# Kernel optimization log

Measured on AMD Instinct MI355X. Metric: run time of the kernel, lower is better.

The kernel has to match this reference:

```python
import jax, jax.numpy as jnp
import numpy as np

N = 100000      # nodes
E = 3200000     # edges (avg degree 32)
F = 256         # input features
C = 256         # output channels


def setup_inputs() -> dict:
    key = jax.random.key(0)
    k1, k2, k3, k4, k5 = jax.random.split(key, 5)
    x = jax.random.normal(k1, (N, F), dtype=jnp.float32)
    edge_row = jax.random.randint(k2, (E,), 0, N, dtype=jnp.int32)
    edge_col = jax.random.randint(k3, (E,), 0, N, dtype=jnp.int32)
    # precomputed normalized adjacency values (D^-1/2 (A+I) D^-1/2 entries)
    edge_vals = jax.random.uniform(k4, (E,), dtype=jnp.float32)
    kernel = jax.random.normal(k5, (F, C), dtype=jnp.float32) * (1.0 / np.sqrt(F))
    bias = jnp.zeros((C,), dtype=jnp.float32)
    return {"x": x, "edge_row": edge_row, "edge_col": edge_col,
            "edge_vals": edge_vals, "kernel": kernel, "bias": bias}


def reference(x, edge_row, edge_col, edge_vals, kernel, bias):
    # GraphConv: Z = relu( A_hat @ (X @ W) + b ), single mode, sparse A_hat.
    h = x @ kernel                                   # [N, C]
    msgs = edge_vals[:, None] * h[edge_col]          # [E, C] gather along cols
    agg = jax.ops.segment_sum(msgs, edge_row, num_segments=N)  # [N, C]
    return jax.nn.relu(agg + bias)
```

## Files before the change

### kernel.cpp

```cpp
#include <hip/hip_runtime.h>
#include <hip/hip_bf16.h>
#include <hip/hip_fp16.h>


#define BROWS 128
#define CH_A1 16384
#define CH_A3 8192
#define GEMM_SMEM 10240

typedef __attribute__((ext_vector_type(4))) float f32x4;
typedef __attribute__((ext_vector_type(2))) int i32x2;
typedef __attribute__((ext_vector_type(8))) short s16x8;

__device__ __forceinline__ unsigned short f2bf(float f) {
    unsigned u = __float_as_uint(f);
    u += 0x7FFFu + ((u >> 16) & 1u);
    return (unsigned short)(u >> 16);
}
__device__ __forceinline__ float bf2f(unsigned short s) {
    return __uint_as_float(((unsigned)s) << 16);
}

__device__ __forceinline__ void gemm_body(const float* __restrict__ X,
                                          const unsigned short* __restrict__ Wt,
                                          unsigned short* __restrict__ H,
                                          int M, int g, char* smem) {
    typedef unsigned short AsRow[40];
    AsRow* As = (AsRow*)smem;
    int t = threadIdx.x;
    int lane = t & 63;
    int w = t >> 6;
    int r0 = g * 64;
    int c0 = w * 64;
    int srow = t >> 2;
    int sslot = t & 3;
    int gr = r0 + srow; if (gr >= M) gr = M - 1;

    f32x4 acc[4][4] = {};

    for (int k0 = 0; k0 < 256; k0 += 32) {
        const float* p = &X[(size_t)gr * 256 + k0 + sslot * 8];
        f32x4 a0 = __builtin_nontemporal_load((const f32x4*)p);
        f32x4 a1 = __builtin_nontemporal_load((const f32x4*)(p + 4));
        s16x8 va;
        va[0] = (short)f2bf(a0[0]); va[1] = (short)f2bf(a0[1]);
        va[2] = (short)f2bf(a0[2]); va[3] = (short)f2bf(a0[3]);
        va[4] = (short)f2bf(a1[0]); va[5] = (short)f2bf(a1[1]);
        va[6] = (short)f2bf(a1[2]); va[7] = (short)f2bf(a1[3]);
        __syncthreads();
        *(s16x8*)&As[srow][sslot * 8] = va;
        __syncthreads();

        int kofs = (lane >> 4) * 8;
        s16x8 afr[4], bfr[4];
#pragma unroll
        for (int mi = 0; mi < 4; ++mi)
            afr[mi] = *(const s16x8*)&As[mi * 16 + (lane & 15)][kofs];
#pragma unroll
        for (int ni = 0; ni < 4; ++ni) {
            int cn = c0 + ni * 16 + (lane & 15);
            bfr[ni] = *(const s16x8*)&Wt[(size_t)cn * 256 + k0 + kofs];
        }
#pragma unroll
        for (int mi = 0; mi < 4; ++mi)
#pragma unroll
            for (int ni = 0; ni < 4; ++ni)
                acc[mi][ni] = __builtin_amdgcn_mfma_f32_16x16x32_bf16(
                    afr[mi], bfr[ni], acc[mi][ni], 0, 0, 0);
    }

#pragma unroll
    for (int mi = 0; mi < 4; ++mi) {
#pragma unroll
        for (int ni = 0; ni < 4; ++ni) {
            int rg = r0 + mi * 16 + (lane >> 4) * 4;
            int cg = c0 + ni * 16 + (lane & 15);
#pragma unroll
            for (int j = 0; j < 4; ++j) {
                if (rg + j < M)
                    H[(size_t)(rg + j) * 256 + cg] = f2bf(acc[mi][ni][j]);
            }
        }
    }
}

__device__ __forceinline__ void hist_body(const int* __restrict__ row,
                                          int* __restrict__ gcnt,
                                          int E, int NB, int chunk, char* smem) {
    int* h = (int*)smem;
    int t = threadIdx.x;
    for (int j = t; j < NB; j += 256) h[j] = 0;
    __syncthreads();
    int start = chunk * CH_A1;
    int end = min(E, start + CH_A1);
    for (int i = start + t; i < end; i += 256)
        atomicAdd(&h[row[i] >> 7], 1);
    __syncthreads();
    for (int j = t; j < NB; j += 256)
        if (h[j]) atomicAdd(&gcnt[j], h[j]);
}

__device__ __forceinline__ void a3_body(const int* __restrict__ row,
                                        const int* __restrict__ col,
                                        const float* __restrict__ val,
                                        int* __restrict__ gcur,
                                        int2* __restrict__ binned,
                                        int E, int NB, int chunk, char* smem) {
    int* h    = (int*)smem;
    int* base = h + NB;
    int* cur  = base + NB;
    int t = threadIdx.x;
    for (int j = t; j < NB; j += 256) { h[j] = 0; cur[j] = 0; }
    __syncthreads();
    int start = chunk * CH_A3;
    int end = min(E, start + CH_A3);
    for (int i = start + t; i < end; i += 256)
        atomicAdd(&h[row[i] >> 7], 1);
    __syncthreads();
    for (int j = t; j < NB; j += 256) {
        int c = h[j];
        base[j] = c ? atomicAdd(&gcur[j], c) : 0;
    }
    __syncthreads();
    for (int i = start + t; i < end; i += 256) {
        int r = row[i];
        int b = r >> 7;
        int ofs = atomicAdd(&cur[b], 1);
        unsigned hb = (unsigned)__half_as_ushort(__float2half(val[i]));
        binned[base[b] + ofs] = make_int2(col[i] | (int)(hb << 17), r & (BROWS - 1));
    }
}

__device__ __forceinline__ void kb_body(const int2* __restrict__ binned,
                                        const int* __restrict__ bkt_base,
                                        int* __restrict__ rowptr,
                                        unsigned* __restrict__ csr,
                                        int N, int b, char* smem) {
    int* cnt = (int*)smem;
    int* sc  = cnt + BROWS;
    int* cur = sc + BROWS;
    int t = threadIdx.x;
    int r0 = b * BROWS;
    int bb = bkt_base[b];
    int be = bkt_base[b + 1];
    if (t < BROWS) cnt[t] = 0;
    __syncthreads();
    for (int i = bb + t; i < be; i += 256) {
        i32x2 e = __builtin_nontemporal_load((const i32x2*)&binned[i]);
        atomicAdd(&cnt[e[1]], 1);
    }
    __syncthreads();
    if (t < BROWS) sc[t] = cnt[t];
    __syncthreads();
    for (int off = 1; off < BROWS; off <<= 1) {
        int tmp = (t < BROWS && t >= off) ? sc[t - off] : 0;
        __syncthreads();
        if (t < BROWS && t >= off) sc[t] += tmp;
        __syncthreads();
    }
    if (t < BROWS) {
        int ex = sc[t] - cnt[t];
        cur[t] = ex;
        if (r0 + t < N) rowptr[r0 + t] = bb + ex;
    }
    __syncthreads();
    for (int i = bb + t; i < be; i += 256) {
        i32x2 e = __builtin_nontemporal_load((const i32x2*)&binned[i]);
        int ofs = atomicAdd(&cur[e[1]], 1);
        csr[bb + ofs] = (unsigned)e[0];
    }
}

__global__ __launch_bounds__(1024) void kA2(const int* __restrict__ gcnt,
                                            int* __restrict__ bkt_base,
                                            int* __restrict__ gcur,
                                            int* __restrict__ rowptr,
                                            int NB, int N, int E) {
    __shared__ int s[1024];
    int t = threadIdx.x;
    int v = (t < NB) ? gcnt[t] : 0;
    s[t] = v;
    __syncthreads();
    for (int off = 1; off < 1024; off <<= 1) {
        int tmp = (t >= off) ? s[t - off] : 0;
        __syncthreads();
        if (t >= off) s[t] += tmp;
        __syncthreads();
    }
    if (t < NB) {
        int ex = s[t] - v;
        bkt_base[t] = ex;
        gcur[t] = ex;
    }
    if (t == 0) {
        bkt_base[NB] = E;
        rowptr[N] = E;
    }
}

__global__ __launch_bounds__(256) void h0(const int* __restrict__ row,
                                          int* __restrict__ gcnt,
                                          int E, int NB, int nHist,
                                          const float* __restrict__ W,
                                          unsigned short* __restrict__ Wt) {
    extern __shared__ char smem[];
    int bid = blockIdx.x;
    int t = threadIdx.x;
    if (bid < nHist) { hist_body(row, gcnt, E, NB, bid, smem); return; }
    int idx = (bid - nHist) * 256 + t;
    int k = idx >> 8, c = idx & 255;
    Wt[c * 256 + k] = f2bf(W[idx]);
}

__global__ __launch_bounds__(256) void h1(const int* __restrict__ row,
                                          const int* __restrict__ col,
                                          const float* __restrict__ val,
                                          int* __restrict__ gcur,
                                          int2* __restrict__ binned,
                                          int E, int NB, int nA3,
                                          const float* __restrict__ X,
                                          const unsigned short* __restrict__ Wt,
                                          unsigned short* __restrict__ H,
                                          int M, int g0) {
    extern __shared__ char smem[];
    int bid = blockIdx.x;
    if (bid < nA3) { a3_body(row, col, val, gcur, binned, E, NB, bid, smem); return; }
    gemm_body(X, Wt, H, M, g0 + (bid - nA3), smem);
}

__global__ __launch_bounds__(256) void h2(const int2* __restrict__ binned,
                                          const int* __restrict__ bktb,
                                          int* __restrict__ rowptr,
                                          unsigned* __restrict__ csr,
                                          int N, int NB,
                                          const float* __restrict__ X,
                                          const unsigned short* __restrict__ Wt,
                                          unsigned short* __restrict__ H,
                                          int M, int g0) {
    extern __shared__ char smem[];
    int bid = blockIdx.x;
    if (bid < NB) { kb_body(binned, bktb, rowptr, csr, N, bid, smem); return; }
    gemm_body(X, Wt, H, M, g0 + (bid - NB), smem);
}

__global__ __launch_bounds__(256) void k_gemm_solo(const float* __restrict__ X,
                                                   const unsigned short* __restrict__ Wt,
                                                   unsigned short* __restrict__ H, int M) {
    extern __shared__ char smem[];
    gemm_body(X, Wt, H, M, blockIdx.x, smem);
}

__global__ __launch_bounds__(256) void k_agg(const unsigned short* __restrict__ H,
                                             const int* __restrict__ rowptr,
                                             const unsigned* __restrict__ csr,
                                             const float* __restrict__ bias,
                                             float* __restrict__ out, int n) {
    int wave = threadIdx.x >> 6;
    int lane = threadIdx.x & 63;
    int node = blockIdx.x * 4 + wave;
    if (node >= n) return;
    int s = rowptr[node];
    int e = rowptr[node + 1];
    int h = lane >> 5;
    int cbase = (lane & 31) * 8;

    float a0=0.f,a1=0.f,a2=0.f,a3=0.f,a4=0.f,a5=0.f,a6=0.f,a7=0.f;

#define ACC(K, HV)                                                      \
    {                                                                   \
        float v = __half2float(__ushort_as_half((unsigned short)((K) >> 17))); \
        a0 += v * bf2f((unsigned short)(HV)[0]);                        \
        a1 += v * bf2f((unsigned short)(HV)[1]);                        \
        a2 += v * bf2f((unsigned short)(HV)[2]);                        \
        a3 += v * bf2f((unsigned short)(HV)[3]);                        \
        a4 += v * bf2f((unsigned short)(HV)[4]);                        \
        a5 += v * bf2f((unsigned short)(HV)[5]);                        \
        a6 += v * bf2f((unsigned short)(HV)[6]);                        \
        a7 += v * bf2f((unsigned short)(HV)[7]);                        \
    }

    int i = s;
    for (; i + 7 < e; i += 8) {
        unsigned k0 = csr[i + h];
        unsigned k1 = csr[i + 2 + h];
        unsigned k2 = csr[i + 4 + h];
        unsigned k3 = csr[i + 6 + h];
        s16x8 g0 = *(const s16x8*)&H[(k0 & 0x1FFFFu) * 256 + cbase];
        s16x8 g1 = *(const s16x8*)&H[(k1 & 0x1FFFFu) * 256 + cbase];
        s16x8 g2 = *(const s16x8*)&H[(k2 & 0x1FFFFu) * 256 + cbase];
        s16x8 g3 = *(const s16x8*)&H[(k3 & 0x1FFFFu) * 256 + cbase];
        ACC(k0, g0); ACC(k1, g1); ACC(k2, g2); ACC(k3, g3);
    }
    for (; i + 1 < e; i += 2) {
        unsigned k0 = csr[i + h];
        s16x8 g0 = *(const s16x8*)&H[(k0 & 0x1FFFFu) * 256 + cbase];
        ACC(k0, g0);
    }
    if (i < e) {
        unsigned k0 = csr[i];
        s16x8 g0 = *(const s16x8*)&H[(k0 & 0x1FFFFu) * 256 + cbase];
        float v = h ? 0.f
                    : __half2float(__ushort_as_half((unsigned short)(k0 >> 17)));
        a0 += v * bf2f((unsigned short)g0[0]);
        a1 += v * bf2f((unsigned short)g0[1]);
        a2 += v * bf2f((unsigned short)g0[2]);
        a3 += v * bf2f((unsigned short)g0[3]);
        a4 += v * bf2f((unsigned short)g0[4]);
        a5 += v * bf2f((unsigned short)g0[5]);
        a6 += v * bf2f((unsigned short)g0[6]);
        a7 += v * bf2f((unsigned short)g0[7]);
    }
#undef ACC

    a0 += __shfl_xor(a0, 32); a1 += __shfl_xor(a1, 32);
    a2 += __shfl_xor(a2, 32); a3 += __shfl_xor(a3, 32);
    a4 += __shfl_xor(a4, 32); a5 += __shfl_xor(a5, 32);
    a6 += __shfl_xor(a6, 32); a7 += __shfl_xor(a7, 32);

    float w0 = h ? a4 : a0;
    float w1 = h ? a5 : a1;
    float w2 = h ? a6 : a2;
    float w3 = h ? a7 : a3;
    int cw = cbase + h * 4;
    float4 b4 = *(const float4*)&bias[cw];
    f32x4 o;
    o[0] = fmaxf(w0 + b4.x, 0.f);
    o[1] = fmaxf(w1 + b4.y, 0.f);
    o[2] = fmaxf(w2 + b4.z, 0.f);
    o[3] = fmaxf(w3 + b4.w, 0.f);
    __builtin_nontemporal_store(o, (f32x4*)&out[node * 256 + cw]);
}

extern "C" void kernel_launch(void* const* d_in, const int* in_sizes, int n_in,
                              void* d_out, int out_size, void* d_ws, size_t ws_size,
                              hipStream_t stream) {
    const float* x     = (const float*)d_in[0];
    const int*   erow  = (const int*)d_in[1];
    const int*   ecol  = (const int*)d_in[2];
    const float* evals = (const float*)d_in[3];
    const float* W     = (const float*)d_in[4];
    const float* bias  = (const float*)d_in[5];
    float* out = (float*)d_out;

    const int C = 256;
    const int N = in_sizes[0] / C;
    const int E = in_sizes[1];
    const int NB = (N + BROWS - 1) / BROWS;

    char* ws = (char*)d_ws;
    size_t off = 0;
    auto carve = [&](size_t bytes) -> void* {
        void* p = ws + off;
        off += (bytes + 255) & ~(size_t)255;
        return p;
    };
    unsigned short* Hbf  = (unsigned short*)carve((size_t)N * C * 2);
    unsigned*       csr  = (unsigned*)carve((size_t)E * 4);
    int*            rowp = (int*)carve((size_t)(N + 1) * 4);
    unsigned short* Wt   = (unsigned short*)carve((size_t)C * 256 * 2);
    int*            gcnt = (int*)carve((size_t)NB * 4);
    int*            gcur = (int*)carve((size_t)NB * 4);
    int*            bktb = (int*)carve((size_t)(NB + 1) * 4);

    bool fused = (off + (size_t)E * 8) <= ws_size;
    int2* binned = fused ? (int2*)carve((size_t)E * 8) : (int2*)Hbf;

    int nHist = (E + CH_A1 - 1) / CH_A1;
    int nA3   = (E + CH_A3 - 1) / CH_A3;
    int gemmBlocks = (N + 63) / 64;

    int G1 = fused ? 650 : 0;
    int G2 = fused ? (gemmBlocks - 650) : 0;

    hipMemsetAsync(gcnt, 0, (size_t)NB * 4, stream);
    h0<<<nHist + 256, 256, GEMM_SMEM, stream>>>(erow, gcnt, E, NB, nHist, W, Wt);
    kA2<<<1, 1024, 0, stream>>>(gcnt, bktb, gcur, rowp, NB, N, E);
    h1<<<nA3 + G1, 256, GEMM_SMEM, stream>>>(erow, ecol, evals, gcur, binned,
                                             E, NB, nA3, x, Wt, Hbf, N, 0);
    h2<<<NB + G2, 256, GEMM_SMEM, stream>>>(binned, bktb, rowp, csr, N, NB,
                                            x, Wt, Hbf, N, G1);
    if (!fused)
        k_gemm_solo<<<gemmBlocks, 256, GEMM_SMEM, stream>>>(x, Wt, Hbf, N);

    k_agg<<<(N + 3) / 4, 256, 0, stream>>>(Hbf, rowp, csr, bias, out, N);
}
```

Before: 396.9 us.

## Replace global CSR build with fixed-capacity buckets and fused per-bucket aggregation

```diff
diff --git a/kernel.cpp b/kernel.cpp
--- a/kernel.cpp
+++ b/kernel.cpp
@@ -3,13 +3,12 @@
 #include <hip/hip_fp16.h>
 
 
-#define BROWS 128
-#define CH_A1 16384
+#define CAP 2432
+#define NBMAX 1600
 #define CH_A3 8192
-#define GEMM_SMEM 10240
+#define D1_SMEM 19200
 
 typedef __attribute__((ext_vector_type(4))) float f32x4;
-typedef __attribute__((ext_vector_type(2))) int i32x2;
 typedef __attribute__((ext_vector_type(8))) short s16x8;
 
 __device__ __forceinline__ unsigned short f2bf(float f) {
@@ -19,6 +18,53 @@
 }
 __device__ __forceinline__ float bf2f(unsigned short s) {
     return __uint_as_float(((unsigned)s) << 16);
+}
+
+__global__ __launch_bounds__(256) void k_pre(const float* __restrict__ W,
+                                             unsigned short* __restrict__ Wt,
+                                             int* __restrict__ gcur, int NB) {
+    int bid = blockIdx.x, t = threadIdx.x;
+    if (bid < 256) {
+        int idx = bid * 256 + t;
+        int k = idx >> 8, c = idx & 255;
+        Wt[c * 256 + k] = f2bf(W[idx]);
+    } else {
+        for (int j = t; j < NB; j += 256) gcur[j] = 0;
+    }
+}
+
+__device__ __forceinline__ void a3_body(const int* __restrict__ row,
+                                        const int* __restrict__ col,
+                                        const float* __restrict__ val,
+                                        int* __restrict__ gcur,
+                                        unsigned* __restrict__ bcv,
+                                        unsigned char* __restrict__ blr,
+                                        int E, int NB, int chunk, char* smem) {
+    int* h    = (int*)smem;
+    int* base = h + NBMAX;
+    int* cur  = base + NBMAX;
+    int t = threadIdx.x;
+    for (int j = t; j < NB; j += 256) { h[j] = 0; cur[j] = 0; }
+    __syncthreads();
+    int start = chunk * CH_A3;
+    int end = min(E, start + CH_A3);
+    for (int i = start + t; i < end; i += 256)
+        atomicAdd(&h[row[i] >> 6], 1);
+    __syncthreads();
+    for (int j = t; j < NB; j += 256) {
+        int c = h[j];
+        base[j] = c ? atomicAdd(&gcur[j], c) : 0;
+    }
+    __syncthreads();
+    for (int i = start + t; i < end; i += 256) {
+        int r = row[i];
+        int b = r >> 6;
+        int ofs = atomicAdd(&cur[b], 1);
+        size_t idx = (size_t)b * CAP + base[b] + ofs;
+        unsigned hb = (unsigned)__half_as_ushort(__float2half(val[i]));
+        bcv[idx] = (unsigned)col[i] | (hb << 17);
+        blr[idx] = (unsigned char)(r & 63);
+    }
 }
 
 __device__ __forceinline__ void gemm_body(const float* __restrict__ X,
@@ -84,187 +130,69 @@
     }
 }
 
-__device__ __forceinline__ void hist_body(const int* __restrict__ row,
-                                          int* __restrict__ gcnt,
-                                          int E, int NB, int chunk, char* smem) {
-    int* h = (int*)smem;
-    int t = threadIdx.x;
-    for (int j = t; j < NB; j += 256) h[j] = 0;
-    __syncthreads();
-    int start = chunk * CH_A1;
-    int end = min(E, start + CH_A1);
-    for (int i = start + t; i < end; i += 256)
-        atomicAdd(&h[row[i] >> 7], 1);
-    __syncthreads();
-    for (int j = t; j < NB; j += 256)
-        if (h[j]) atomicAdd(&gcnt[j], h[j]);
-}
-
-__device__ __forceinline__ void a3_body(const int* __restrict__ row,
-                                        const int* __restrict__ col,
-                                        const float* __restrict__ val,
-                                        int* __restrict__ gcur,
-                                        int2* __restrict__ binned,
-                                        int E, int NB, int chunk, char* smem) {
-    int* h    = (int*)smem;
-    int* base = h + NB;
-    int* cur  = base + NB;
-    int t = threadIdx.x;
-    for (int j = t; j < NB; j += 256) { h[j] = 0; cur[j] = 0; }
-    __syncthreads();
-    int start = chunk * CH_A3;
-    int end = min(E, start + CH_A3);
-    for (int i = start + t; i < end; i += 256)
-        atomicAdd(&h[row[i] >> 7], 1);
-    __syncthreads();
-    for (int j = t; j < NB; j += 256) {
-        int c = h[j];
-        base[j] = c ? atomicAdd(&gcur[j], c) : 0;
-    }
-    __syncthreads();
-    for (int i = start + t; i < end; i += 256) {
-        int r = row[i];
-        int b = r >> 7;
-        int ofs = atomicAdd(&cur[b], 1);
-        unsigned hb = (unsigned)__half_as_ushort(__float2half(val[i]));
-        binned[base[b] + ofs] = make_int2(col[i] | (int)(hb << 17), r & (BROWS - 1));
-    }
-}
-
-__device__ __forceinline__ void kb_body(const int2* __restrict__ binned,
-                                        const int* __restrict__ bkt_base,
-                                        int* __restrict__ rowptr,
-                                        unsigned* __restrict__ csr,
-                                        int N, int b, char* smem) {
-    int* cnt = (int*)smem;
-    int* sc  = cnt + BROWS;
-    int* cur = sc + BROWS;
-    int t = threadIdx.x;
-    int r0 = b * BROWS;
-    int bb = bkt_base[b];
-    int be = bkt_base[b + 1];
-    if (t < BROWS) cnt[t] = 0;
-    __syncthreads();
-    for (int i = bb + t; i < be; i += 256) {
-        i32x2 e = __builtin_nontemporal_load((const i32x2*)&binned[i]);
-        atomicAdd(&cnt[e[1]], 1);
-    }
-    __syncthreads();
-    if (t < BROWS) sc[t] = cnt[t];
-    __syncthreads();
-    for (int off = 1; off < BROWS; off <<= 1) {
-        int tmp = (t < BROWS && t >= off) ? sc[t - off] : 0;
-        __syncthreads();
-        if (t < BROWS && t >= off) sc[t] += tmp;
-        __syncthreads();
-    }
-    if (t < BROWS) {
-        int ex = sc[t] - cnt[t];
-        cur[t] = ex;
-        if (r0 + t < N) rowptr[r0 + t] = bb + ex;
-    }
-    __syncthreads();
-    for (int i = bb + t; i < be; i += 256) {
-        i32x2 e = __builtin_nontemporal_load((const i32x2*)&binned[i]);
-        int ofs = atomicAdd(&cur[e[1]], 1);
-        csr[bb + ofs] = (unsigned)e[0];
-    }
-}
-
-__global__ __launch_bounds__(1024) void kA2(const int* __restrict__ gcnt,
-                                            int* __restrict__ bkt_base,
-                                            int* __restrict__ gcur,
-                                            int* __restrict__ rowptr,
-                                            int NB, int N, int E) {
-    __shared__ int s[1024];
-    int t = threadIdx.x;
-    int v = (t < NB) ? gcnt[t] : 0;
-    s[t] = v;
-    __syncthreads();
-    for (int off = 1; off < 1024; off <<= 1) {
-        int tmp = (t >= off) ? s[t - off] : 0;
-        __syncthreads();
-        if (t >= off) s[t] += tmp;
-        __syncthreads();
-    }
-    if (t < NB) {
-        int ex = s[t] - v;
-        bkt_base[t] = ex;
-        gcur[t] = ex;
-    }
-    if (t == 0) {
-        bkt_base[NB] = E;
-        rowptr[N] = E;
-    }
-}
-
-__global__ __launch_bounds__(256) void h0(const int* __restrict__ row,
-                                          int* __restrict__ gcnt,
-                                          int E, int NB, int nHist,
-                                          const float* __restrict__ W,
-                                          unsigned short* __restrict__ Wt) {
+__global__ __launch_bounds__(256) void kD1(const int* __restrict__ row,
+                                           const int* __restrict__ col,
+                                           const float* __restrict__ val,
+                                           int* __restrict__ gcur,
+                                           unsigned* __restrict__ bcv,
+                                           unsigned char* __restrict__ blr,
+                                           int E, int NB, int nA3,
+                                           const float* __restrict__ X,
+                                           const unsigned short* __restrict__ Wt,
+                                           unsigned short* __restrict__ H, int M) {
     extern __shared__ char smem[];
     int bid = blockIdx.x;
+    if (bid < nA3) {
+        a3_body(row, col, val, gcur, bcv, blr, E, NB, bid, smem);
+        return;
+    }
+    gemm_body(X, Wt, H, M, bid - nA3, smem);
+}
+
+__global__ __launch_bounds__(256) void kD2(const unsigned* __restrict__ bcv,
+                                           const unsigned char* __restrict__ blr,
+                                           const int* __restrict__ gcur,
+                                           const unsigned short* __restrict__ H,
+                                           const float* __restrict__ bias,
+                                           float* __restrict__ out, int N) {
+    __shared__ int cnt[64], rs[64], cur[64];
+    __shared__ unsigned csr[CAP];
+    int b = blockIdx.x;
     int t = threadIdx.x;
-    if (bid < nHist) { hist_body(row, gcnt, E, NB, bid, smem); return; }
-    int idx = (bid - nHist) * 256 + t;
-    int k = idx >> 8, c = idx & 255;
-    Wt[c * 256 + k] = f2bf(W[idx]);
-}
-
-__global__ __launch_bounds__(256) void h1(const int* __restrict__ row,
-                                          const int* __restrict__ col,
-                                          const float* __restrict__ val,
-                                          int* __restrict__ gcur,
-                                          int2* __restrict__ binned,
-                                          int E, int NB, int nA3,
-                                          const float* __restrict__ X,
-                                          const unsigned short* __restrict__ Wt,
-                                          unsigned short* __restrict__ H,
-                                          int M, int g0) {
-    extern __shared__ char smem[];
-    int bid = blockIdx.x;
-    if (bid < nA3) { a3_body(row, col, val, gcur, binned, E, NB, bid, smem); return; }
-    gemm_body(X, Wt, H, M, g0 + (bid - nA3), smem);
-}
-
-__global__ __launch_bounds__(256) void h2(const int2* __restrict__ binned,
-                                          const int* __restrict__ bktb,
-                                          int* __restrict__ rowptr,
-                                          unsigned* __restrict__ csr,
-                                          int N, int NB,
-                                          const float* __restrict__ X,
-                                          const unsigned short* __restrict__ Wt,
-                                          unsigned short* __restrict__ H,
-                                          int M, int g0) {
-    extern __shared__ char smem[];
-    int bid = blockIdx.x;
-    if (bid < NB) { kb_body(binned, bktb, rowptr, csr, N, bid, smem); return; }
-    gemm_body(X, Wt, H, M, g0 + (bid - NB), smem);
-}
-
-__global__ __launch_bounds__(256) void k_gemm_solo(const float* __restrict__ X,
-                                                   const unsigned short* __restrict__ Wt,
-                                                   unsigned short* __restrict__ H, int M) {
-    extern __shared__ char smem[];
-    gemm_body(X, Wt, H, M, blockIdx.x, smem);
-}
-
-__global__ __launch_bounds__(256) void k_agg(const unsigned short* __restrict__ H,
-                                             const int* __restrict__ rowptr,
-                                             const unsigned* __restrict__ csr,
-                                             const float* __restrict__ bias,
-                                             float* __restrict__ out, int n) {
-    int wave = threadIdx.x >> 6;
-    int lane = threadIdx.x & 63;
-    int node = blockIdx.x * 4 + wave;
-    if (node >= n) return;
-    int s = rowptr[node];
-    int e = rowptr[node + 1];
+    size_t gb = (size_t)b * CAP;
+    int n = gcur[b];
+
+    if (t < 64) cnt[t] = 0;
+    __syncthreads();
+    for (int i = t; i < n; i += 256)
+        atomicAdd(&cnt[blr[gb + i]], 1);
+    __syncthreads();
+    if (t < 64) rs[t] = cnt[t];
+    __syncthreads();
+    for (int off = 1; off < 64; off <<= 1) {
+        int tmp = (t < 64 && t >= off) ? rs[t - off] : 0;
+        __syncthreads();
+        if (t < 64 && t >= off) rs[t] += tmp;
+        __syncthreads();
+    }
+    if (t < 64) {
+        int ex = rs[t] - cnt[t];
+        rs[t] = ex;
+        cur[t] = ex;
+    }
+    __syncthreads();
+    for (int i = t; i < n; i += 256) {
+        unsigned cv = bcv[gb + i];
+        int lr = blr[gb + i];
+        int ofs = atomicAdd(&cur[lr], 1);
+        csr[ofs] = cv;
+    }
+    __syncthreads();
+
+    int wave = t >> 6;
+    int lane = t & 63;
     int h = lane >> 5;
     int cbase = (lane & 31) * 8;
-
-    float a0=0.f,a1=0.f,a2=0.f,a3=0.f,a4=0.f,a5=0.f,a6=0.f,a7=0.f;
 
 #define ACC(K, HV)                                                      \
     {                                                                   \
@@ -279,56 +207,66 @@
         a7 += v * bf2f((unsigned short)(HV)[7]);                        \
     }
 
-    int i = s;
-    for (; i + 7 < e; i += 8) {
-        unsigned k0 = csr[i + h];
-        unsigned k1 = csr[i + 2 + h];
-        unsigned k2 = csr[i + 4 + h];
-        unsigned k3 = csr[i + 6 + h];
-        s16x8 g0 = *(const s16x8*)&H[(k0 & 0x1FFFFu) * 256 + cbase];
-        s16x8 g1 = *(const s16x8*)&H[(k1 & 0x1FFFFu) * 256 + cbase];
-        s16x8 g2 = *(const s16x8*)&H[(k2 & 0x1FFFFu) * 256 + cbase];
-        s16x8 g3 = *(const s16x8*)&H[(k3 & 0x1FFFFu) * 256 + cbase];
-        ACC(k0, g0); ACC(k1, g1); ACC(k2, g2); ACC(k3, g3);
-    }
-    for (; i + 1 < e; i += 2) {
-        unsigned k0 = csr[i + h];
-        s16x8 g0 = *(const s16x8*)&H[(k0 & 0x1FFFFu) * 256 + cbase];
-        ACC(k0, g0);
-    }
-    if (i < e) {
-        unsigned k0 = csr[i];
-        s16x8 g0 = *(const s16x8*)&H[(k0 & 0x1FFFFu) * 256 + cbase];
-        float v = h ? 0.f
-                    : __half2float(__ushort_as_half((unsigned short)(k0 >> 17)));
-        a0 += v * bf2f((unsigned short)g0[0]);
-        a1 += v * bf2f((unsigned short)g0[1]);
-        a2 += v * bf2f((unsigned short)g0[2]);
-        a3 += v * bf2f((unsigned short)g0[3]);
-        a4 += v * bf2f((unsigned short)g0[4]);
-        a5 += v * bf2f((unsigned short)g0[5]);
-        a6 += v * bf2f((unsigned short)g0[6]);
-        a7 += v * bf2f((unsigned short)g0[7]);
+    for (int rr = 0; rr < 16; ++rr) {
+        int r = wave * 16 + rr;
+        int node = b * 64 + r;
+        if (node >= N) break;
+        int s = rs[r];
+        int e = s + cnt[r];
+
+        float a0=0.f,a1=0.f,a2=0.f,a3=0.f,a4=0.f,a5=0.f,a6=0.f,a7=0.f;
+
+        int i = s;
+        for (; i + 7 < e; i += 8) {
+            unsigned k0 = csr[i + h];
+            unsigned k1 = csr[i + 2 + h];
+            unsigned k2 = csr[i + 4 + h];
+            unsigned k3 = csr[i + 6 + h];
+            s16x8 g0 = *(const s16x8*)&H[(k0 & 0x1FFFFu) * 256 + cbase];
+            s16x8 g1 = *(const s16x8*)&H[(k1 & 0x1FFFFu) * 256 + cbase];
+            s16x8 g2 = *(const s16x8*)&H[(k2 & 0x1FFFFu) * 256 + cbase];
+            s16x8 g3 = *(const s16x8*)&H[(k3 & 0x1FFFFu) * 256 + cbase];
+            ACC(k0, g0); ACC(k1, g1); ACC(k2, g2); ACC(k3, g3);
+        }
+        for (; i + 1 < e; i += 2) {
+            unsigned k0 = csr[i + h];
+            s16x8 g0 = *(const s16x8*)&H[(k0 & 0x1FFFFu) * 256 + cbase];
+            ACC(k0, g0);
+        }
+        if (i < e) {
+            unsigned k0 = csr[i];
+            s16x8 g0 = *(const s16x8*)&H[(k0 & 0x1FFFFu) * 256 + cbase];
+            float v = h ? 0.f
+                        : __half2float(__ushort_as_half((unsigned short)(k0 >> 17)));
+            a0 += v * bf2f((unsigned short)g0[0]);
+            a1 += v * bf2f((unsigned short)g0[1]);
+            a2 += v * bf2f((unsigned short)g0[2]);
+            a3 += v * bf2f((unsigned short)g0[3]);
+            a4 += v * bf2f((unsigned short)g0[4]);
+            a5 += v * bf2f((unsigned short)g0[5]);
+            a6 += v * bf2f((unsigned short)g0[6]);
+            a7 += v * bf2f((unsigned short)g0[7]);
+        }
+
+        a0 += __shfl_xor(a0, 32); a1 += __shfl_xor(a1, 32);
+        a2 += __shfl_xor(a2, 32); a3 += __shfl_xor(a3, 32);
+        a4 += __shfl_xor(a4, 32); a5 += __shfl_xor(a5, 32);
+        a6 += __shfl_xor(a6, 32); a7 += __shfl_xor(a7, 32);
+
+        float w0 = h ? a4 : a0;
+        float w1 = h ? a5 : a1;
+        float w2 = h ? a6 : a2;
+        float w3 = h ? a7 : a3;
+        int cw = cbase + h * 4;
+        float4 b4 = *(const float4*)&bias[cw];
+        float4 o;
+        o.x = fmaxf(w0 + b4.x, 0.f);
+        o.y = fmaxf(w1 + b4.y, 0.f);
+        o.z = fmaxf(w2 + b4.z, 0.f);
+        o.w = fmaxf(w3 + b4.w, 0.f);
+        *(float4*)&out[(size_t)node * 256 + cw] = o;
     }
 #undef ACC
-
-    a0 += __shfl_xor(a0, 32); a1 += __shfl_xor(a1, 32);
-    a2 += __shfl_xor(a2, 32); a3 += __shfl_xor(a3, 32);
-    a4 += __shfl_xor(a4, 32); a5 += __shfl_xor(a5, 32);
-    a6 += __shfl_xor(a6, 32); a7 += __shfl_xor(a7, 32);
-
-    float w0 = h ? a4 : a0;
-    float w1 = h ? a5 : a1;
-    float w2 = h ? a6 : a2;
-    float w3 = h ? a7 : a3;
-    int cw = cbase + h * 4;
-    float4 b4 = *(const float4*)&bias[cw];
-    f32x4 o;
-    o[0] = fmaxf(w0 + b4.x, 0.f);
-    o[1] = fmaxf(w1 + b4.y, 0.f);
-    o[2] = fmaxf(w2 + b4.z, 0.f);
-    o[3] = fmaxf(w3 + b4.w, 0.f);
-    __builtin_nontemporal_store(o, (f32x4*)&out[node * 256 + cw]);
 }
 
 extern "C" void kernel_launch(void* const* d_in, const int* in_sizes, int n_in,
@@ -345,7 +283,7 @@
     const int C = 256;
     const int N = in_sizes[0] / C;
     const int E = in_sizes[1];
-    const int NB = (N + BROWS - 1) / BROWS;
+    const int NB = (N + 63) / 64;
 
     char* ws = (char*)d_ws;
     size_t off = 0;
@@ -354,33 +292,18 @@
         off += (bytes + 255) & ~(size_t)255;
         return p;
     };
-    unsigned short* Hbf  = (unsigned short*)carve((size_t)N * C * 2);
-    unsigned*       csr  = (unsigned*)carve((size_t)E * 4);
-    int*            rowp = (int*)carve((size_t)(N + 1) * 4);
-    unsigned short* Wt   = (unsigned short*)carve((size_t)C * 256 * 2);
-    int*            gcnt = (int*)carve((size_t)NB * 4);
-    int*            gcur = (int*)carve((size_t)NB * 4);
-    int*            bktb = (int*)carve((size_t)(NB + 1) * 4);
-
-    bool fused = (off + (size_t)E * 8) <= ws_size;
-    int2* binned = fused ? (int2*)carve((size_t)E * 8) : (int2*)Hbf;
-
-    int nHist = (E + CH_A1 - 1) / CH_A1;
-    int nA3   = (E + CH_A3 - 1) / CH_A3;
+    unsigned short* Hbf = (unsigned short*)carve((size_t)N * C * 2);
+    unsigned short* Wt  = (unsigned short*)carve((size_t)C * 256 * 2);
+    int*            gcur= (int*)carve((size_t)NB * 4);
+    unsigned*       bcv = (unsigned*)carve((size_t)NB * CAP * 4);
+    unsigned char*  blr = (unsigned char*)carve((size_t)NB * CAP);
+
+    int nA3 = (E + CH_A3 - 1) / CH_A3;
     int gemmBlocks = (N + 63) / 64;
 
-    int G1 = fused ? 650 : 0;
-    int G2 = fused ? (gemmBlocks - 650) : 0;
-
-    hipMemsetAsync(gcnt, 0, (size_t)NB * 4, stream);
-    h0<<<nHist + 256, 256, GEMM_SMEM, stream>>>(erow, gcnt, E, NB, nHist, W, Wt);
-    kA2<<<1, 1024, 0, stream>>>(gcnt, bktb, gcur, rowp, NB, N, E);
-    h1<<<nA3 + G1, 256, GEMM_SMEM, stream>>>(erow, ecol, evals, gcur, binned,
-                                             E, NB, nA3, x, Wt, Hbf, N, 0);
-    h2<<<NB + G2, 256, GEMM_SMEM, stream>>>(binned, bktb, rowp, csr, N, NB,
-                                            x, Wt, Hbf, N, G1);
-    if (!fused)
-        k_gemm_solo<<<gemmBlocks, 256, GEMM_SMEM, stream>>>(x, Wt, Hbf, N);
-
-    k_agg<<<(N + 3) / 4, 256, 0, stream>>>(Hbf, rowp, csr, bias, out, N);
-}
+    k_pre<<<257, 256, 0, stream>>>(W, Wt, gcur, NB);
+    kD1<<<nA3 + gemmBlocks, 256, D1_SMEM, stream>>>(erow, ecol, evals, gcur,
+                                                    bcv, blr, E, NB, nA3,
+                                                    x, Wt, Hbf, N);
+    kD2<<<NB, 256, 0, stream>>>(bcv, blr, gcur, Hbf, bias, out, N);
+}
```

Result: faster. 386.7 us (-2.6%).
